# Performance work log

Measured on AMD Instinct MI355X. Metric: run time of the kernel, lower is better.

## Reference

```python
import jax, jax.numpy as jnp
import numpy as np

# dims: batch, spatial H x W, channels-last
B, H, W = 16, 256, 256
CIN, COUT = 32, 32
N_MODES = (32, 32)
EM0 = N_MODES[0] // 2        # 16 (eff modes along first spatial dim)
EM1 = N_MODES[1] // 2 + 1    # 17 (eff modes along last rfft dim)
WF = W // 2 + 1              # 129 rfft bins


def setup_inputs() -> dict:
    key = jax.random.key(0)
    kx, k1r, k1i, k2r, k2i, kb = jax.random.split(key, 6)
    wshape = (CIN, COUT, EM0, EM1)
    # variance-scaling-ish scale: scale=0.5, fan_avg
    wscale = np.float32(np.sqrt(0.5 / ((CIN + COUT) / 2.0)))
    return {
        "x": jax.random.normal(kx, (B, H, W, CIN), dtype=jnp.float32),
        "w1_real": jax.random.normal(k1r, wshape, dtype=jnp.float32) * wscale,
        "w1_imag": jax.random.normal(k1i, wshape, dtype=jnp.float32) * wscale,
        "w2_real": jax.random.normal(k2r, wshape, dtype=jnp.float32) * wscale,
        "w2_imag": jax.random.normal(k2i, wshape, dtype=jnp.float32) * wscale,
        "bias": jax.random.normal(kb, (1, 1, 1, COUT), dtype=jnp.float32) * 0.1,
    }


def reference(x, w1_real, w1_imag, w2_real, w2_imag, bias):
    # forward-normalized real FFT over the two spatial axes: (B,H,WF,CIN) complex64
    x_ft = jnp.fft.rfftn(x, axes=(1, 2), norm="forward")
    w1 = w1_real + 1j * w1_imag  # corner signs=(+1,): low rows
    w2 = w2_real + 1j * w2_imag  # corner signs=(-1,): high (negative-freq) rows
    # per-corner complex mode mixing: contract input channels -> output channels
    top = jnp.einsum("bhwi,iohw->bhwo", x_ft[:, :EM0, :EM1, :], w1)
    bot = jnp.einsum("bhwi,iohw->bhwo", x_ft[:, -EM0:, :EM1, :], w2)
    out_ft = jnp.zeros((B, H, WF, COUT), dtype=jnp.complex64)
    out_ft = out_ft.at[:, :EM0, :EM1, :].set(top)
    out_ft = out_ft.at[:, -EM0:, :EM1, :].set(bot)
    y = jnp.fft.irfftn(out_ft, s=(H, W), axes=(1, 2), norm="forward")
    return y + bias
```

## Files before the change

### kernel.cpp

```cpp
#include <hip/hip_runtime.h>

#define NB 16
#define NH 256
#define EM1 17
#define TWO_PI 6.283185307179586f

__device__ __forceinline__ void cmul_upd(float& tr, float& ti, float wr, float wi) {
    float nr = tr * wr - ti * wi;
    float ni = tr * wi + ti * wr;
    tr = nr; ti = ni;
}

__global__ __launch_bounds__(256) void k1_fwdW(const float* __restrict__ x,
                                               float2* __restrict__ Xw) {
    __shared__ __align__(16) float xs[4 * 64 * 32];
    const int t = threadIdx.x;
    const int r = t >> 6;
    const int l = t & 63;
    const int g = l >> 3;
    const int cg = l & 7;
    const int row = blockIdx.x * 4 + r;
    const int b = row >> 8, y = row & 255;

    float wc0, ws0, wc1, ws1;
    sincosf(-TWO_PI * (float)g * (1.f / 256.f), &ws0, &wc0);
    sincosf(-TWO_PI * (float)(g + 8) * (1.f / 256.f), &ws1, &wc1);
    float t0r = 1.f, t0i = 0.f, t1r = 1.f, t1i = 0.f;
    float a0r[4] = {0,0,0,0}, a0i[4] = {0,0,0,0};
    float a1r[4] = {0,0,0,0}, a1i[4] = {0,0,0,0};
    float pr[4]  = {0,0,0,0}, pq[4]  = {0,0,0,0};

    const float K16C[8] = {1.f, 0.92387953251f, 0.70710678119f, 0.38268343236f,
                           0.f, -0.38268343236f, -0.70710678119f, -0.92387953251f};
    const float K16S[8] = {0.f, -0.38268343236f, -0.70710678119f, -0.92387953251f,
                           -1.f, -0.92387953251f, -0.70710678119f, -0.38268343236f};

    const float4* gsrc = (const float4*)(x + (size_t)blockIdx.x * 32768);

    #pragma unroll 1
    for (int c = 0; c < 4; ++c) {
        __syncthreads();
        #pragma unroll
        for (int q = 0; q < 8; ++q) {
            int v = q * 256 + t;
            int rr = v >> 9, id = v & 511;
            ((float4*)xs)[v] = gsrc[(size_t)rr * 2048 + c * 512 + id];
        }
        __syncthreads();
        const float* xp = xs + r * 2048 + cg * 4;
        #pragma unroll
        for (int xx = 0; xx < 64; ++xx) {
            float4 v = *(const float4*)(xp + xx * 32);
            float vv[4] = {v.x, v.y, v.z, v.w};
            #pragma unroll
            for (int k = 0; k < 4; ++k) {
                a0r[k] = fmaf(vv[k], t0r, a0r[k]);
                a0i[k] = fmaf(vv[k], t0i, a0i[k]);
                a1r[k] = fmaf(vv[k], t1r, a1r[k]);
                a1i[k] = fmaf(vv[k], t1i, a1i[k]);
            }
            cmul_upd(t0r, t0i, wc0, ws0);
            cmul_upd(t1r, t1i, wc1, ws1);
        }
        const float* kp = xs + r * 2048 + g * 256 + cg * 4;
        #pragma unroll
        for (int j = 0; j < 8; ++j) {
            float4 v = *(const float4*)(kp + j * 32);
            float vv[4] = {v.x, v.y, v.z, v.w};
            const float cj = K16C[j], sj = K16S[j];
            #pragma unroll
            for (int k = 0; k < 4; ++k) {
                pr[k] = fmaf(vv[k], cj, pr[k]);
                pq[k] = fmaf(vv[k], sj, pq[k]);
            }
        }
    }

    const float sc = 1.0f / 65536.0f;
    size_t base0 = (((size_t)b * 17 + g) * 256 + y) * 32 + cg * 4;
    *(float4*)(Xw + base0)     = make_float4(a0r[0]*sc, a0i[0]*sc, a0r[1]*sc, a0i[1]*sc);
    *(float4*)(Xw + base0 + 2) = make_float4(a0r[2]*sc, a0i[2]*sc, a0r[3]*sc, a0i[3]*sc);
    size_t base1 = (((size_t)b * 17 + g + 8) * 256 + y) * 32 + cg * 4;
    *(float4*)(Xw + base1)     = make_float4(a1r[0]*sc, a1i[0]*sc, a1r[1]*sc, a1i[1]*sc);
    *(float4*)(Xw + base1 + 2) = make_float4(a1r[2]*sc, a1i[2]*sc, a1r[3]*sc, a1i[3]*sc);

    float sg = (g & 1) ? -1.f : 1.f;
    #pragma unroll
    for (int k = 0; k < 4; ++k) { pr[k] *= sg; pq[k] *= sg; }
    #pragma unroll
    for (int m = 8; m <= 32; m <<= 1) {
        #pragma unroll
        for (int k = 0; k < 4; ++k) {
            pr[k] += __shfl_xor(pr[k], m);
            pq[k] += __shfl_xor(pq[k], m);
        }
    }
    if (g == 0) {
        size_t b16 = (((size_t)b * 17 + 16) * 256 + y) * 32 + cg * 4;
        *(float4*)(Xw + b16)     = make_float4(pr[0]*sc, pq[0]*sc, pr[1]*sc, pq[1]*sc);
        *(float4*)(Xw + b16 + 2) = make_float4(pr[2]*sc, pq[2]*sc, pr[3]*sc, pq[3]*sc);
    }
}

__global__ __launch_bounds__(256) void k2_fwdH(const float2* __restrict__ Xw,
                                               float2* __restrict__ xft) {
    __shared__ __align__(16) float2 xsh[256 * 16];
    const int t = threadIdx.x;
    const int bk = blockIdx.x;
    const int b = bk / 34;
    const int rem = bk - b * 34;
    const int kw = rem >> 1, ih = rem & 1;
    const float2* src = Xw + ((size_t)(b * 17 + kw) * 256) * 32 + ih * 16;
    #pragma unroll
    for (int q = 0; q < 8; ++q) {
        int v = q * 256 + t;
        int yy = v >> 3, quad = v & 7;
        ((float4*)xsh)[v] = *(const float4*)(src + (size_t)yy * 32 + quad * 2);
    }
    __syncthreads();
    const int m = t & 31, ip = t >> 5;
    const int kh = (m < 16) ? m : m - 32;
    float wc, ws; sincosf(-TWO_PI * (float)kh * (1.f / 256.f), &ws, &wc);
    float tr = 1.f, ti = 0.f;
    float a0r = 0.f, a0i = 0.f, a1r = 0.f, a1i = 0.f;
    const float* xp = (const float*)xsh + ip * 4;
    #pragma unroll 8
    for (int yy = 0; yy < 256; ++yy) {
        float4 v = *(const float4*)(xp + yy * 32);
        a0r = fmaf(v.x, tr, a0r); a0r = fmaf(-v.y, ti, a0r);
        a0i = fmaf(v.x, ti, a0i); a0i = fmaf(v.y, tr, a0i);
        a1r = fmaf(v.z, tr, a1r); a1r = fmaf(-v.w, ti, a1r);
        a1i = fmaf(v.z, ti, a1i); a1i = fmaf(v.w, tr, a1i);
        cmul_upd(tr, ti, wc, ws);
    }
    size_t o = ((size_t)b * 32 + m) * 544 + (size_t)kw * 32 + ih * 16 + ip * 2;
    *(float4*)(xft + o) = make_float4(a0r, a0i, a1r, a1i);
}

__global__ __launch_bounds__(256) void k3_mix(const float2* __restrict__ xft,
                                              const float* __restrict__ w1r,
                                              const float* __restrict__ w1i,
                                              const float* __restrict__ w2r,
                                              const float* __restrict__ w2i,
                                              float2* __restrict__ oft) {
    __shared__ float wrl[1024];
    __shared__ float wil[1024];
    __shared__ float2 xbl[512];
    int bk = blockIdx.x;
    int m = bk / 17, kw = bk - m * 17;
    const float* wr_g; const float* wi_g; int h;
    if (m < 16) { wr_g = w1r; wi_g = w1i; h = m; }
    else        { wr_g = w2r; wi_g = w2i; h = m - 16; }
    int t = threadIdx.x;
#pragma unroll
    for (int c = 0; c < 4; ++c) {
        int u = (c << 8) + t;
        int ii = u >> 5, o = u & 31;
        size_t gi = ((size_t)(ii * 32 + o) * 16 + h) * 17 + kw;
        wrl[u] = wr_g[gi]; wil[u] = wi_g[gi];
    }
#pragma unroll
    for (int c = 0; c < 2; ++c) {
        int u = (c << 8) + t;
        int bb = u >> 5, ii = u & 31;
        xbl[u] = xft[(size_t)bb * 17408 + (size_t)m * 544 + (size_t)kw * 32 + ii];
    }
    __syncthreads();
    int o = t & 31, bg = t >> 5;
#pragma unroll
    for (int rr = 0; rr < 2; ++rr) {
        int bb = bg + 8 * rr;
        float ar = 0.f, ai = 0.f;
#pragma unroll
        for (int ii = 0; ii < 32; ++ii) {
            float2 xv = xbl[bb * 32 + ii];
            float wr_ = wrl[ii * 32 + o], wi_ = wil[ii * 32 + o];
            ar = fmaf(xv.x, wr_, ar); ar = fmaf(-xv.y, wi_, ar);
            ai = fmaf(xv.x, wi_, ai); ai = fmaf(xv.y, wr_, ai);
        }
        oft[(size_t)bb * 17408 + (size_t)m * 544 + (size_t)kw * 32 + o] =
            make_float2(ar, ai);
    }
}

__global__ __launch_bounds__(256) void k4_invH(const float2* __restrict__ oft,
                                               float2* __restrict__ T) {
    __shared__ __align__(16) float2 ol[32 * 16];
    const int t = threadIdx.x;
    const int bk = blockIdx.x;
    const int b = bk / 34;
    const int rem = bk - b * 34;
    const int kw = rem >> 1, oh = rem & 1;
    {
        int mm = t >> 3, quad = t & 7;
        ((float4*)ol)[t] = *(const float4*)(oft + (size_t)b * 17408 +
                                            (size_t)mm * 544 + (size_t)kw * 32 + oh * 16 + quad * 2);
    }
    __syncthreads();
    const int y = t;
    float uc, us; sincosf(TWO_PI * (float)y * (1.f / 256.f), &us, &uc);
    float tr = 1.f, ti = 0.f;
    float ar[16], ai[16];
    #pragma unroll
    for (int o = 0; o < 16; ++o) { ar[o] = 0.f; ai[o] = 0.f; }
    for (int m = 0; m < 32; ++m) {
        if (m == 16) ti = -ti;
        #pragma unroll
        for (int o2 = 0; o2 < 8; ++o2) {
            float4 v = *(const float4*)((const float*)ol + m * 32 + o2 * 4);
            int o = o2 * 2;
            ar[o]   = fmaf(v.x, tr, ar[o]);   ar[o]   = fmaf(-v.y, ti, ar[o]);
            ai[o]   = fmaf(v.x, ti, ai[o]);   ai[o]   = fmaf(v.y, tr, ai[o]);
            ar[o+1] = fmaf(v.z, tr, ar[o+1]); ar[o+1] = fmaf(-v.w, ti, ar[o+1]);
            ai[o+1] = fmaf(v.z, ti, ai[o+1]); ai[o+1] = fmaf(v.w, tr, ai[o+1]);
        }
        cmul_upd(tr, ti, uc, us);
    }
    float2* dst = T + ((size_t)(b * 256 + y) * 17 + kw) * 32 + oh * 16;
    #pragma unroll
    for (int o2 = 0; o2 < 8; ++o2) {
        *(float4*)(dst + o2 * 2) =
            make_float4(ar[o2*2], ai[o2*2], ar[o2*2+1], ai[o2*2+1]);
    }
}

__global__ __launch_bounds__(256) void k5_invW(const float2* __restrict__ T,
                                               const float* __restrict__ bias,
                                               float* __restrict__ out) {
    __shared__ __align__(16) float2 tl[544];
    __shared__ float bl[32];
    const int t = threadIdx.x;
    const int blk = blockIdx.x;
    const float4* src4 = (const float4*)(T + (size_t)blk * 544);
    for (int u = t; u < 272; u += 256) ((float4*)tl)[u] = src4[u];
    if (t < 32) bl[t] = bias[t];
    __syncthreads();
    const int o8 = t & 3, xq = t >> 2;
    float c0, s0; sincosf(TWO_PI * (float)(xq * 4) * (1.f / 256.f), &s0, &c0);
    const float CC = 0.99969881869620422f, SS = 0.02454122852291229f;
    float ur[4], ui[4];
    ur[0] = c0; ui[0] = s0;
    #pragma unroll
    for (int k = 1; k < 4; ++k) {
        ur[k] = ur[k-1] * CC - ui[k-1] * SS;
        ui[k] = ur[k-1] * SS + ui[k-1] * CC;
    }
    float tr_[4], ti_[4];
    #pragma unroll
    for (int k = 0; k < 4; ++k) { tr_[k] = ur[k]; ti_[k] = ui[k]; }
    float acc[4][8];
    #pragma unroll
    for (int k = 0; k < 4; ++k)
        #pragma unroll
        for (int o = 0; o < 8; ++o) acc[k][o] = 0.f;
    #pragma unroll 4
    for (int kw = 1; kw < 17; ++kw) {
        #pragma unroll
        for (int o2 = 0; o2 < 4; ++o2) {
            float4 v = *(const float4*)((const float*)tl + kw * 64 + o8 * 16 + o2 * 4);
            #pragma unroll
            for (int k = 0; k < 4; ++k) {
                acc[k][o2*2]   = fmaf(v.x, tr_[k], acc[k][o2*2]);
                acc[k][o2*2]   = fmaf(-v.y, ti_[k], acc[k][o2*2]);
                acc[k][o2*2+1] = fmaf(v.z, tr_[k], acc[k][o2*2+1]);
                acc[k][o2*2+1] = fmaf(-v.w, ti_[k], acc[k][o2*2+1]);
            }
        }
        #pragma unroll
        for (int k = 0; k < 4; ++k) cmul_upd(tr_[k], ti_[k], ur[k], ui[k]);
    }
    float base[8];
    #pragma unroll
    for (int o = 0; o < 8; ++o) {
        int og = o8 * 8 + o;
        base[o] = tl[og].x + bl[og];
    }
    float* orow = out + (size_t)blk * 8192;
    #pragma unroll
    for (int k = 0; k < 4; ++k) {
        int xx = xq * 4 + k;
        float res[8];
        #pragma unroll
        for (int o = 0; o < 8; ++o) res[o] = fmaf(2.f, acc[k][o], base[o]);
        float* dst = orow + xx * 32 + o8 * 8;
        *(float4*)(dst)     = make_float4(res[0], res[1], res[2], res[3]);
        *(float4*)(dst + 4) = make_float4(res[4], res[5], res[6], res[7]);
    }
}

extern "C" void kernel_launch(void* const* d_in, const int* in_sizes, int n_in,
                              void* d_out, int out_size, void* d_ws, size_t ws_size,
                              hipStream_t stream) {
    const float* x    = (const float*)d_in[0];
    const float* w1r  = (const float*)d_in[1];
    const float* w1i  = (const float*)d_in[2];
    const float* w2r  = (const float*)d_in[3];
    const float* w2i  = (const float*)d_in[4];
    const float* bias = (const float*)d_in[5];
    float* out = (float*)d_out;

    char* ws = (char*)d_ws;
    float2* Xw  = (float2*)ws;
    float2* T   = Xw;
    float2* xft = (float2*)(ws + 17825792);
    float2* oft = (float2*)(ws + 17825792 + 2228224);

    k1_fwdW<<<NB * NH / 4, 256, 0, stream>>>(x, Xw);
    k2_fwdH<<<NB * EM1 * 2, 256, 0, stream>>>(Xw, xft);
    k3_mix <<<32 * EM1, 256, 0, stream>>>(xft, w1r, w1i, w2r, w2i, oft);
    k4_invH<<<NB * EM1 * 2, 256, 0, stream>>>(oft, T);
    k5_invW<<<NB * NH, 256, 0, stream>>>(T, bias, out);
}
```

Before: 326.8 us.

## Compute forward W-axis partial DFT with split-bf16 MFMA matrix multiplies

Replaces the scalar FMA-based forward DFT along W (first 17 rfft bins) with a matrix multiply on MFMA units. Each input row is split into bf16 hi/lo parts in LDS, and a precomputed cos/sin DFT matrix, also split hi/lo and held in registers, is used for three-term bf16 MFMAs that approximate fp32 accuracy. Each block now handles 8 rows with 512 blocks. The risks are reduced precision from the bf16 split, strided scalar global loads and stores, and extra conversion work.

```diff
diff --git a/kernel.cpp b/kernel.cpp
--- a/kernel.cpp
+++ b/kernel.cpp
@@ -5,100 +5,119 @@
 #define EM1 17
 #define TWO_PI 6.283185307179586f
 
+typedef short short8 __attribute__((ext_vector_type(8)));
+typedef float floatx4 __attribute__((ext_vector_type(4)));
+
+__device__ __forceinline__ unsigned f2b(float x){ union{float f; unsigned u;} v; v.f=x; return v.u; }
+__device__ __forceinline__ float b2f(unsigned u){ union{float f; unsigned u;} v; v.u=u; return v.f; }
+
 __device__ __forceinline__ void cmul_upd(float& tr, float& ti, float wr, float wi) {
     float nr = tr * wr - ti * wi;
     float ni = tr * wi + ti * wr;
     tr = nr; ti = ni;
 }
 
-__global__ __launch_bounds__(256) void k1_fwdW(const float* __restrict__ x,
-                                               float2* __restrict__ Xw) {
-    __shared__ __align__(16) float xs[4 * 64 * 32];
+__global__ __launch_bounds__(256, 2) void k1_fwdW_mfma(const float* __restrict__ x,
+                                                       float* __restrict__ Xw) {
+    __shared__ __align__(16) short alds[16384];
     const int t = threadIdx.x;
-    const int r = t >> 6;
+    const int w = t >> 6;
     const int l = t & 63;
-    const int g = l >> 3;
-    const int cg = l & 7;
-    const int row = blockIdx.x * 4 + r;
-    const int b = row >> 8, y = row & 255;
-
-    float wc0, ws0, wc1, ws1;
-    sincosf(-TWO_PI * (float)g * (1.f / 256.f), &ws0, &wc0);
-    sincosf(-TWO_PI * (float)(g + 8) * (1.f / 256.f), &ws1, &wc1);
-    float t0r = 1.f, t0i = 0.f, t1r = 1.f, t1i = 0.f;
-    float a0r[4] = {0,0,0,0}, a0i[4] = {0,0,0,0};
-    float a1r[4] = {0,0,0,0}, a1i[4] = {0,0,0,0};
-    float pr[4]  = {0,0,0,0}, pq[4]  = {0,0,0,0};
-
-    const float K16C[8] = {1.f, 0.92387953251f, 0.70710678119f, 0.38268343236f,
-                           0.f, -0.38268343236f, -0.70710678119f, -0.92387953251f};
-    const float K16S[8] = {0.f, -0.38268343236f, -0.70710678119f, -0.92387953251f,
-                           -1.f, -0.92387953251f, -0.70710678119f, -0.38268343236f};
-
-    const float4* gsrc = (const float4*)(x + (size_t)blockIdx.x * 32768);
-
-    #pragma unroll 1
-    for (int c = 0; c < 4; ++c) {
+    const int mt = w & 1;
+    const int g  = w >> 1;
+    const int nn = (g == 0) ? 2 : 1;
+
+    short8 Bh[2][8], Bl[2][8];
+    const float sc = 1.0f / 65536.0f;
+    #pragma unroll
+    for (int u = 0; u < 2; ++u) {
+        const int nt  = (g == 0) ? u : 2;
+        const int n   = nt * 16 + (l & 15);
+        const int kwv = n >> 1;
+        const int par = n & 1;
+        const bool live = (u < nn) && (n < 34);
+        const float dth = (TWO_PI / 256.f) * (float)kwv;
+        #pragma unroll
+        for (int ks = 0; ks < 8; ++ks) {
+            const int k0 = ks * 32 + (l >> 4) * 8;
+            float s, c; sincosf(dth * (float)k0, &s, &c);
+            float sd, cd; sincosf(dth, &sd, &cd);
+            short8 vh, vl;
+            #pragma unroll
+            for (int j = 0; j < 8; ++j) {
+                float v = live ? ((par ? -s : c) * sc) : 0.f;
+                unsigned ub = f2b(v);
+                short h16 = (short)(ub >> 16);
+                float rres = v - b2f(ub & 0xFFFF0000u);
+                short l16 = (short)(f2b(rres) >> 16);
+                vh[j] = h16; vl[j] = l16;
+                float ncv = c * cd - s * sd, nsv = c * sd + s * cd;
+                c = ncv; s = nsv;
+            }
+            Bh[u][ks] = vh; Bl[u][ks] = vl;
+        }
+    }
+
+    const int i   = t & 31;
+    const int slot = t >> 5;
+    const int i15 = i & 15, imt = i >> 4;
+    const int i15l = l & 15, ql = l >> 4;
+
+    for (int ir = 0; ir < 8; ++ir) {
+        const int row = blockIdx.x * 8 + ir;
+        const int b = row >> 8, y = row & 255;
         __syncthreads();
-        #pragma unroll
-        for (int q = 0; q < 8; ++q) {
-            int v = q * 256 + t;
-            int rr = v >> 9, id = v & 511;
-            ((float4*)xs)[v] = gsrc[(size_t)rr * 2048 + c * 512 + id];
+        {
+            const float* rp = x + (size_t)row * 8192;
+            unsigned* al32 = (unsigned*)alds;
+            #pragma unroll
+            for (int c = 0; c < 16; ++c) {
+                const int xp = slot + (c << 3);
+                float v0 = rp[xp * 64 + i];
+                float v1 = rp[xp * 64 + 32 + i];
+                unsigned u0 = f2b(v0), u1 = f2b(v1);
+                unsigned hi = (u0 >> 16) | (u1 & 0xFFFF0000u);
+                float r0 = v0 - b2f(u0 & 0xFFFF0000u);
+                float r1 = v1 - b2f(u1 & 0xFFFF0000u);
+                unsigned lo = (f2b(r0) >> 16) | (f2b(r1) & 0xFFFF0000u);
+                const int ks = xp >> 4, q = (xp & 15) >> 2, dw = xp & 3;
+                const int base = (ks * 2 + imt) * 256 + (q * 16 + i15) * 4 + dw;
+                al32[base] = hi;
+                al32[base + 16 * 256] = lo;
+            }
         }
         __syncthreads();
-        const float* xp = xs + r * 2048 + cg * 4;
-        #pragma unroll
-        for (int xx = 0; xx < 64; ++xx) {
-            float4 v = *(const float4*)(xp + xx * 32);
-            float vv[4] = {v.x, v.y, v.z, v.w};
-            #pragma unroll
-            for (int k = 0; k < 4; ++k) {
-                a0r[k] = fmaf(vv[k], t0r, a0r[k]);
-                a0i[k] = fmaf(vv[k], t0i, a0i[k]);
-                a1r[k] = fmaf(vv[k], t1r, a1r[k]);
-                a1i[k] = fmaf(vv[k], t1i, a1i[k]);
-            }
-            cmul_upd(t0r, t0i, wc0, ws0);
-            cmul_upd(t1r, t1i, wc1, ws1);
-        }
-        const float* kp = xs + r * 2048 + g * 256 + cg * 4;
-        #pragma unroll
-        for (int j = 0; j < 8; ++j) {
-            float4 v = *(const float4*)(kp + j * 32);
-            float vv[4] = {v.x, v.y, v.z, v.w};
-            const float cj = K16C[j], sj = K16S[j];
-            #pragma unroll
-            for (int k = 0; k < 4; ++k) {
-                pr[k] = fmaf(vv[k], cj, pr[k]);
-                pq[k] = fmaf(vv[k], sj, pq[k]);
-            }
-        }
-    }
-
-    const float sc = 1.0f / 65536.0f;
-    size_t base0 = (((size_t)b * 17 + g) * 256 + y) * 32 + cg * 4;
-    *(float4*)(Xw + base0)     = make_float4(a0r[0]*sc, a0i[0]*sc, a0r[1]*sc, a0i[1]*sc);
-    *(float4*)(Xw + base0 + 2) = make_float4(a0r[2]*sc, a0i[2]*sc, a0r[3]*sc, a0i[3]*sc);
-    size_t base1 = (((size_t)b * 17 + g + 8) * 256 + y) * 32 + cg * 4;
-    *(float4*)(Xw + base1)     = make_float4(a1r[0]*sc, a1i[0]*sc, a1r[1]*sc, a1i[1]*sc);
-    *(float4*)(Xw + base1 + 2) = make_float4(a1r[2]*sc, a1i[2]*sc, a1r[3]*sc, a1i[3]*sc);
-
-    float sg = (g & 1) ? -1.f : 1.f;
-    #pragma unroll
-    for (int k = 0; k < 4; ++k) { pr[k] *= sg; pq[k] *= sg; }
-    #pragma unroll
-    for (int m = 8; m <= 32; m <<= 1) {
-        #pragma unroll
-        for (int k = 0; k < 4; ++k) {
-            pr[k] += __shfl_xor(pr[k], m);
-            pq[k] += __shfl_xor(pq[k], m);
-        }
-    }
-    if (g == 0) {
-        size_t b16 = (((size_t)b * 17 + 16) * 256 + y) * 32 + cg * 4;
-        *(float4*)(Xw + b16)     = make_float4(pr[0]*sc, pq[0]*sc, pr[1]*sc, pq[1]*sc);
-        *(float4*)(Xw + b16 + 2) = make_float4(pr[2]*sc, pq[2]*sc, pr[3]*sc, pq[3]*sc);
+        floatx4 acc0 = {0.f, 0.f, 0.f, 0.f};
+        floatx4 acc1 = {0.f, 0.f, 0.f, 0.f};
+        #pragma unroll
+        for (int ks = 0; ks < 8; ++ks) {
+            const short8 ah = *(const short8*)(alds + ((ks * 2 + mt) * 512) + l * 8);
+            const short8 al = *(const short8*)(alds + ((16 + ks * 2 + mt) * 512) + l * 8);
+            acc0 = __builtin_amdgcn_mfma_f32_16x16x32_bf16(ah, Bh[0][ks], acc0, 0, 0, 0);
+            acc0 = __builtin_amdgcn_mfma_f32_16x16x32_bf16(ah, Bl[0][ks], acc0, 0, 0, 0);
+            acc0 = __builtin_amdgcn_mfma_f32_16x16x32_bf16(al, Bh[0][ks], acc0, 0, 0, 0);
+            if (nn == 2) {
+                acc1 = __builtin_amdgcn_mfma_f32_16x16x32_bf16(ah, Bh[1][ks], acc1, 0, 0, 0);
+                acc1 = __builtin_amdgcn_mfma_f32_16x16x32_bf16(ah, Bl[1][ks], acc1, 0, 0, 0);
+                acc1 = __builtin_amdgcn_mfma_f32_16x16x32_bf16(al, Bh[1][ks], acc1, 0, 0, 0);
+            }
+        }
+        #pragma unroll
+        for (int u = 0; u < 2; ++u) {
+            if (u >= nn) break;
+            const int nt = (g == 0) ? u : 2;
+            const int n = nt * 16 + i15l;
+            if (n < 34) {
+                const int kwv = n >> 1, par = n & 1;
+                float* dst = Xw + (((size_t)(b * 17 + kwv) * 256 + y) * 64) + par;
+                const floatx4 a = (u == 0) ? acc0 : acc1;
+                #pragma unroll
+                for (int r = 0; r < 4; ++r) {
+                    const int ii = mt * 16 + ql * 4 + r;
+                    dst[ii * 2] = a[r];
+                }
+            }
+        }
     }
 }
 
@@ -305,7 +324,7 @@
     float2* xft = (float2*)(ws + 17825792);
     float2* oft = (float2*)(ws + 17825792 + 2228224);
 
-    k1_fwdW<<<NB * NH / 4, 256, 0, stream>>>(x, Xw);
+    k1_fwdW_mfma<<<512, 256, 0, stream>>>(x, (float*)Xw);
     k2_fwdH<<<NB * EM1 * 2, 256, 0, stream>>>(Xw, xft);
     k3_mix <<<32 * EM1, 256, 0, stream>>>(xft, w1r, w1i, w2r, w2i, oft);
     k4_invH<<<NB * EM1 * 2, 256, 0, stream>>>(oft, T);
```

New measurement: 315.1 us. 1.04x faster.
